# Optimization experiments

Measured on AMD Instinct MI355X. Metric: run time of the kernel, lower is better.

## Reference

```python
import jax, jax.numpy as jnp
import numpy as np


def setup_inputs() -> dict:
    key = jax.random.key(0)
    k1, k2, k3 = jax.random.split(key, 3)
    Bt, N, Fin, Fout = 16, 4096, 1024, 1024
    X = jax.random.normal(k1, (Bt, N, Fin), dtype=jnp.float32)
    B = jax.random.normal(k2, (Fin, Fout), dtype=jnp.float32) * (1.0 / np.sqrt(Fin))
    cT = jax.random.normal(k3, (1, Fout), dtype=jnp.float32) * (1.0 / np.sqrt(Fin))
    return {"X": X, "B": B, "cT": cT}


def reference(X, B, cT):
    # Original computes (1/N) * (o1 @ o1.T) @ X @ B + o1 @ cT,
    # which is mathematically mean(X, axis=-2) @ B + cT broadcast to all N rows.
    N = X.shape[-2]
    mean = jnp.mean(X, axis=-2, keepdims=True)          # [..., 1, Fin]
    row = mean @ B + cT                                  # [..., 1, Fout]
    return jnp.broadcast_to(row, X.shape[:-1] + (B.shape[1],))
```

## Files before the change

### kernel.cpp

```cpp
#include <hip/hip_runtime.h>

#define BT   16
#define NR   4096
#define FIN  1024
#define FOUT 1024

#define NCHUNK 64
#define ROWS_PER_CHUNK (NR / NCHUNK)
#define ROWS_PER_BLOCK 32

__global__ void colsum_partial(const float* __restrict__ X, float* __restrict__ part) {
    const int rc = blockIdx.x;
    const int b  = blockIdx.y;
    const int t  = threadIdx.x;
    const float4* src = reinterpret_cast<const float4*>(
        X + (size_t)b * NR * FIN + (size_t)rc * ROWS_PER_CHUNK * FIN) + t;
    float4 a0 = {0.f, 0.f, 0.f, 0.f};
    float4 a1 = {0.f, 0.f, 0.f, 0.f};
#pragma unroll 4
    for (int r = 0; r < ROWS_PER_CHUNK; r += 2) {
        float4 v0 = src[(size_t)r       * (FIN / 4)];
        float4 v1 = src[(size_t)(r + 1) * (FIN / 4)];
        a0.x += v0.x; a0.y += v0.y; a0.z += v0.z; a0.w += v0.w;
        a1.x += v1.x; a1.y += v1.y; a1.z += v1.z; a1.w += v1.w;
    }
    float4 acc = {a0.x + a1.x, a0.y + a1.y, a0.z + a1.z, a0.w + a1.w};
    reinterpret_cast<float4*>(part + ((size_t)b * NCHUNK + rc) * FIN)[t] = acc;
}

__global__ void matvec_fused(const float* __restrict__ part, const float* __restrict__ Bm,
                             const float* __restrict__ cT, float* __restrict__ row) {
    const int foc = blockIdx.x;
    const int b   = blockIdx.y;
    const int t   = threadIdx.x;
    __shared__ float sm[FIN];
    __shared__ float red[4][64];
    {
        const float4* src = reinterpret_cast<const float4*>(part + (size_t)b * NCHUNK * FIN) + t;
        float4 a = {0.f, 0.f, 0.f, 0.f};
#pragma unroll 8
        for (int c = 0; c < NCHUNK; ++c) {
            float4 v = src[(size_t)c * (FIN / 4)];
            a.x += v.x; a.y += v.y; a.z += v.z; a.w += v.w;
        }
        const float inv = 1.0f / (float)NR;
        reinterpret_cast<float4*>(sm)[t] = make_float4(a.x * inv, a.y * inv, a.z * inv, a.w * inv);
    }
    __syncthreads();
    const int fo_idx = t & 63;
    const int g      = t >> 6;
    const int fo     = foc * 64 + fo_idx;
    const float* bp  = Bm + (size_t)(g * 256) * FOUT + fo;
    float f0 = 0.f, f1 = 0.f;
#pragma unroll 8
    for (int k = 0; k < 256; k += 2) {
        f0 += sm[g * 256 + k]     * bp[(size_t)k       * FOUT];
        f1 += sm[g * 256 + k + 1] * bp[(size_t)(k + 1) * FOUT];
    }
    red[g][fo_idx] = f0 + f1;
    __syncthreads();
    if (g == 0) {
        float r = red[0][fo_idx] + red[1][fo_idx] + red[2][fo_idx] + red[3][fo_idx] + cT[fo];
        row[(size_t)b * FOUT + fo] = r;
    }
}

__global__ void bcast_rows(const float* __restrict__ row, float* __restrict__ out) {
    const int rc = blockIdx.x;
    const int b  = blockIdx.y;
    const int t  = threadIdx.x;
    const float4 v = reinterpret_cast<const float4*>(row + (size_t)b * FOUT)[t];
    float4* dst = reinterpret_cast<float4*>(
        out + (size_t)b * NR * FOUT + (size_t)rc * ROWS_PER_BLOCK * FOUT) + t;
#pragma unroll 8
    for (int r = 0; r < ROWS_PER_BLOCK; ++r) {
        dst[(size_t)r * (FOUT / 4)] = v;
    }
}

extern "C" void kernel_launch(void* const* d_in, const int* in_sizes, int n_in,
                              void* d_out, int out_size, void* d_ws, size_t ws_size,
                              hipStream_t stream) {
    const float* X  = (const float*)d_in[0];
    const float* Bm = (const float*)d_in[1];
    const float* cT = (const float*)d_in[2];
    float* out = (float*)d_out;

    float* part = (float*)d_ws;
    float* row  = part + (size_t)BT * NCHUNK * FIN;

    colsum_partial<<<dim3(NCHUNK, BT), 256, 0, stream>>>(X, part);
    matvec_fused<<<dim3(FOUT / 64, BT), 256, 0, stream>>>(part, Bm, cT, row);
    bcast_rows<<<dim3(NR / ROWS_PER_BLOCK, BT), 256, 0, stream>>>(row, out);
}
```

Before: 467.0 us.

## Use grid-stride flat column-sum and broadcast with nontemporal loads and stores

Replaces the per-chunk column-sum and per-row-block broadcast kernels with flat grid-stride kernels. Each thread sweeps strided float4 elements using nontemporal loads and stores so streaming traffic bypasses cache retention. The partial count grows to 128 chunks, which enlarges the workspace read by the matvec stage. The broadcast holds all 16 batch rows in registers per thread, which raises register pressure.

```diff
diff --git a/kernel.cpp b/kernel.cpp
--- a/kernel.cpp
+++ b/kernel.cpp
@@ -5,27 +5,32 @@
 #define FIN  1024
 #define FOUT 1024
 
-#define NCHUNK 64
-#define ROWS_PER_CHUNK (NR / NCHUNK)
-#define ROWS_PER_BLOCK 32
+#define NCHUNK 128
+#define CS_BLOCKS 128
+#define CS_STRIDE (CS_BLOCKS * 256)
+#define CS_ITERS  ((NR * FIN / 4) / CS_STRIDE)
 
-__global__ void colsum_partial(const float* __restrict__ X, float* __restrict__ part) {
-    const int rc = blockIdx.x;
+#define BC_BLOCKS 1024
+#define BC_STRIDE (BC_BLOCKS * 256)
+#define BC_ITERS  ((BT * NR * FIN / 4) / BC_STRIDE)
+
+typedef float f32x4 __attribute__((ext_vector_type(4)));
+
+__global__ void colsum_flat(const float* __restrict__ X, float* __restrict__ part) {
     const int b  = blockIdx.y;
-    const int t  = threadIdx.x;
-    const float4* src = reinterpret_cast<const float4*>(
-        X + (size_t)b * NR * FIN + (size_t)rc * ROWS_PER_CHUNK * FIN) + t;
-    float4 a0 = {0.f, 0.f, 0.f, 0.f};
-    float4 a1 = {0.f, 0.f, 0.f, 0.f};
-#pragma unroll 4
-    for (int r = 0; r < ROWS_PER_CHUNK; r += 2) {
-        float4 v0 = src[(size_t)r       * (FIN / 4)];
-        float4 v1 = src[(size_t)(r + 1) * (FIN / 4)];
-        a0.x += v0.x; a0.y += v0.y; a0.z += v0.z; a0.w += v0.w;
-        a1.x += v1.x; a1.y += v1.y; a1.z += v1.z; a1.w += v1.w;
+    const int bt = blockIdx.x * 256 + threadIdx.x;
+    const f32x4* src = reinterpret_cast<const f32x4*>(X + (size_t)b * NR * FIN) + bt;
+    f32x4 a0 = {0.f, 0.f, 0.f, 0.f};
+    f32x4 a1 = {0.f, 0.f, 0.f, 0.f};
+#pragma unroll
+    for (int i = 0; i < CS_ITERS; i += 2) {
+        f32x4 v0 = __builtin_nontemporal_load(&src[(size_t)i * CS_STRIDE]);
+        f32x4 v1 = __builtin_nontemporal_load(&src[(size_t)(i + 1) * CS_STRIDE]);
+        a0 += v0;
+        a1 += v1;
     }
-    float4 acc = {a0.x + a1.x, a0.y + a1.y, a0.z + a1.z, a0.w + a1.w};
-    reinterpret_cast<float4*>(part + ((size_t)b * NCHUNK + rc) * FIN)[t] = acc;
+    f32x4 acc = a0 + a1;
+    reinterpret_cast<f32x4*>(part)[((size_t)b * NCHUNK + (bt >> 8)) * (FIN / 4) + (bt & 255)] = acc;
 }
 
 __global__ void matvec_fused(const float* __restrict__ part, const float* __restrict__ Bm,
@@ -36,15 +41,15 @@
     __shared__ float sm[FIN];
     __shared__ float red[4][64];
     {
-        const float4* src = reinterpret_cast<const float4*>(part + (size_t)b * NCHUNK * FIN) + t;
-        float4 a = {0.f, 0.f, 0.f, 0.f};
+        const f32x4* src = reinterpret_cast<const f32x4*>(part) + (size_t)b * NCHUNK * (FIN / 4) + t;
+        f32x4 a = {0.f, 0.f, 0.f, 0.f};
 #pragma unroll 8
         for (int c = 0; c < NCHUNK; ++c) {
-            float4 v = src[(size_t)c * (FIN / 4)];
-            a.x += v.x; a.y += v.y; a.z += v.z; a.w += v.w;
+            a += src[(size_t)c * (FIN / 4)];
         }
         const float inv = 1.0f / (float)NR;
-        reinterpret_cast<float4*>(sm)[t] = make_float4(a.x * inv, a.y * inv, a.z * inv, a.w * inv);
+        a *= inv;
+        reinterpret_cast<f32x4*>(sm)[t] = a;
     }
     __syncthreads();
     const int fo_idx = t & 63;
@@ -65,16 +70,17 @@
     }
 }
 
-__global__ void bcast_rows(const float* __restrict__ row, float* __restrict__ out) {
-    const int rc = blockIdx.x;
-    const int b  = blockIdx.y;
-    const int t  = threadIdx.x;
-    const float4 v = reinterpret_cast<const float4*>(row + (size_t)b * FOUT)[t];
-    float4* dst = reinterpret_cast<float4*>(
-        out + (size_t)b * NR * FOUT + (size_t)rc * ROWS_PER_BLOCK * FOUT) + t;
-#pragma unroll 8
-    for (int r = 0; r < ROWS_PER_BLOCK; ++r) {
-        dst[(size_t)r * (FOUT / 4)] = v;
+__global__ void bcast_flat(const float* __restrict__ row, float* __restrict__ out) {
+    const int tid = blockIdx.x * 256 + threadIdx.x;
+    const int c4  = tid & 255;
+    f32x4 v[BT];
+#pragma unroll
+    for (int b = 0; b < BT; ++b)
+        v[b] = reinterpret_cast<const f32x4*>(row + (size_t)b * FOUT)[c4];
+    f32x4* dst = reinterpret_cast<f32x4*>(out) + tid;
+#pragma unroll
+    for (int i = 0; i < BC_ITERS; ++i) {
+        __builtin_nontemporal_store(v[i >> 2], &dst[(size_t)i * BC_STRIDE]);
     }
 }
 
@@ -89,7 +95,7 @@
     float* part = (float*)d_ws;
     float* row  = part + (size_t)BT * NCHUNK * FIN;
 
-    colsum_partial<<<dim3(NCHUNK, BT), 256, 0, stream>>>(X, part);
+    colsum_flat<<<dim3(CS_BLOCKS, BT), 256, 0, stream>>>(X, part);
     matvec_fused<<<dim3(FOUT / 64, BT), 256, 0, stream>>>(part, Bm, cT, row);
-    bcast_rows<<<dim3(NR / ROWS_PER_BLOCK, BT), 256, 0, stream>>>(row, out);
+    bcast_flat<<<dim3(BC_BLOCKS), 256, 0, stream>>>(row, out);
 }
```

New measurement: 454.3 us. -2.7%, faster.
